# Performance work log

Measured on AMD Instinct MI355X. Metric: run time of the kernel, lower is better.

## Reference

```python
import jax, jax.numpy as jnp
import numpy as np

NEG_SLOPE = 0.2  # PyG GATConv default negative_slope
N_NODES = 50000


def gat_conv(x, src, dst, W, att_src, att_dst, bias, heads, out_ch):
    # x: [N, F_in]; src/dst: [E] (messages flow src -> dst, softmax over dst)
    N = x.shape[0]
    h = (x @ W).reshape(N, heads, out_ch)              # [N,H,C]
    a_src = jnp.sum(h * att_src, axis=-1)              # [N,H]
    a_dst = jnp.sum(h * att_dst, axis=-1)              # [N,H]
    e = jax.nn.leaky_relu(a_src[src] + a_dst[dst], NEG_SLOPE)   # [E,H]
    # numerically stable segment softmax over incoming edges of each dst node
    m = jax.ops.segment_max(e, dst, num_segments=N)    # [N,H]
    e = jnp.exp(e - m[dst])
    denom = jax.ops.segment_sum(e, dst, num_segments=N)
    alpha = e / (denom[dst] + 1e-16)                   # [E,H]
    msg = h[src] * alpha[:, :, None]                   # [E,H,C]
    out = jax.ops.segment_sum(msg, dst, num_segments=N)  # [N,H,C]
    return out.reshape(N, heads * out_ch) + bias


def add_self_loops(edge_index, num_nodes):
    loop = jnp.arange(num_nodes, dtype=edge_index.dtype)
    return jnp.concatenate([edge_index, jnp.stack([loop, loop])], axis=1)


def setup_inputs() -> dict:
    key = jax.random.key(0)
    ks = jax.random.split(key, 10)
    F_in, H, C, F_out = 256, 4, 64, 16
    x = jax.random.normal(ks[0], (N_NODES, F_in), dtype=jnp.float32)
    edge_index = jax.random.randint(ks[1], (2, 800000), 0, N_NODES, dtype=jnp.int64)
    s1 = 1.0 / np.sqrt(F_in)
    s2 = 1.0 / np.sqrt(H * C)
    return {
        "x": x,
        "edge_index": edge_index,
        "W1": jax.random.normal(ks[2], (F_in, H * C), dtype=jnp.float32) * s1,
        "att_src1": jax.random.normal(ks[3], (H, C), dtype=jnp.float32) * s2,
        "att_dst1": jax.random.normal(ks[4], (H, C), dtype=jnp.float32) * s2,
        "b1": jnp.zeros((H * C,), dtype=jnp.float32),
        "W2": jax.random.normal(ks[5], (H * C, F_out), dtype=jnp.float32) * s2,
        "att_src2": jax.random.normal(ks[6], (1, F_out), dtype=jnp.float32) * 0.25,
        "att_dst2": jax.random.normal(ks[7], (1, F_out), dtype=jnp.float32) * 0.25,
        "b2": jnp.zeros((F_out,), dtype=jnp.float32),
    }


def reference(x, edge_index, W1, att_src1, att_dst1, b1, W2, att_src2, att_dst2, b2):
    ei = add_self_loops(edge_index, x.shape[0])
    src, dst = ei[0], ei[1]
    H1, C1 = att_src1.shape
    h = gat_conv(x, src, dst, W1, att_src1, att_dst1, b1, H1, C1)
    h = jax.nn.relu(h)
    # F.dropout(training=False) is identity in eval mode
    H2, C2 = att_src2.shape
    out = gat_conv(h, src, dst, W2, att_src2, att_dst2, b2, H2, C2)
    return jax.nn.log_softmax(out, axis=1)
```

## Files before the change

kernel.cpp:

```cpp
#include <hip/hip_runtime.h>
#include <math.h>


typedef __attribute__((ext_vector_type(8))) short bf16x8;
typedef __attribute__((ext_vector_type(8))) unsigned short u16x8;
typedef __attribute__((ext_vector_type(4))) float f32x4;
typedef __attribute__((ext_vector_type(2))) float f32x2;

static __device__ inline unsigned short f2bf(float f) {
    unsigned u = __builtin_bit_cast(unsigned, f);
    unsigned r = (u + 0x7FFF + ((u >> 16) & 1)) >> 16;
    return (unsigned short)r;
}
static __device__ inline float bf2f(unsigned short u) {
    unsigned v = ((unsigned)u) << 16;
    return __builtin_bit_cast(float, v);
}
static __device__ inline float lrelu(float x) { return x > 0.f ? x : 0.2f * x; }

__global__ __launch_bounds__(256) void k_prep(const float* __restrict__ x,
                                              const float* __restrict__ W1,
                                              const float* __restrict__ b1,
                                              const float* __restrict__ W2,
                                              short* __restrict__ xb,
                                              unsigned short* __restrict__ csr,
                                              short* __restrict__ w1t,
                                              float* __restrict__ b1p,
                                              float* __restrict__ w2p,
                                              int* __restrict__ cnt,
                                              float* __restrict__ a1s,
                                              float* __restrict__ a2s,
                                              unsigned* __restrict__ h1f8u,
                                              float* __restrict__ h2,
                                              int N) {
    long idx = (long)blockIdx.x * 256 + threadIdx.x;
    const long T = (long)N * 32;
    if (idx < T) {
        const float* xp = x + idx * 8;
        float4 f0 = *(const float4*)xp;
        float4 f1 = *(const float4*)(xp + 4);
        short b[8];
        b[0] = (short)f2bf(f0.x); b[1] = (short)f2bf(f0.y);
        b[2] = (short)f2bf(f0.z); b[3] = (short)f2bf(f0.w);
        b[4] = (short)f2bf(f1.x); b[5] = (short)f2bf(f1.y);
        b[6] = (short)f2bf(f1.z); b[7] = (short)f2bf(f1.w);
        *(bf16x8*)(xb + idx * 8) = *(bf16x8*)&b[0];
    }
    if (idx < (long)N * 16) {
        ushort4 v = make_ushort4((unsigned short)N, (unsigned short)N,
                                 (unsigned short)N, (unsigned short)N);
        if ((idx & 15) == 0) v.x = (unsigned short)(idx >> 4);
        *(ushort4*)(csr + idx * 4) = v;
    }
    if (idx < N) cnt[idx] = 1;
    if (idx < 256) {
        int ct = ((int)idx >> 6) * 64 + ((int)idx & 3) * 16 + (((int)idx & 63) >> 2);
        b1p[idx] = b1[ct];
    }
    if (idx < 4096) {
        int pp = (int)idx >> 4, c2 = (int)idx & 15;
        int ct = (pp >> 6) * 64 + (pp & 3) * 16 + ((pp & 63) >> 2);
        w2p[idx] = W2[ct * 16 + c2];
    }
    if (idx < 4) a1s[(long)N * 4 + idx] = -1e30f;
    if (idx == 4) a2s[N] = -1e30f;
    if (idx < 64) h1f8u[(long)N * 64 + idx] = 0u;
    if (idx < 16) h2[(long)N * 16 + idx] = 0.f;
    if (idx < 65536) {
        int n = (int)idx >> 8, k = (int)idx & 255;
        w1t[n * 256 + k] = (short)f2bf(W1[k * 256 + n]);
    }
}

__global__ __launch_bounds__(256) void k_scatter(const int* __restrict__ ei,
                                                 int* __restrict__ cnt,
                                                 unsigned short* __restrict__ csr,
                                                 int E0) {
    int e0 = (blockIdx.x * 256 + threadIdx.x) << 3;
    if (e0 >= E0) return;
    if (e0 + 8 <= E0) {
        int4 sa = *(const int4*)&ei[e0];
        int4 sb = *(const int4*)&ei[e0 + 4];
        int4 da = *(const int4*)&ei[E0 + e0];
        int4 db = *(const int4*)&ei[E0 + e0 + 4];
        int ss[8] = {sa.x, sa.y, sa.z, sa.w, sb.x, sb.y, sb.z, sb.w};
        int dd[8] = {da.x, da.y, da.z, da.w, db.x, db.y, db.z, db.w};
        int sl[8];
#pragma unroll
        for (int q = 0; q < 8; ++q) sl[q] = atomicAdd(&cnt[dd[q]], 1);
#pragma unroll
        for (int q = 0; q < 8; ++q)
            if (sl[q] < 64) csr[((long)dd[q] << 6) + sl[q]] = (unsigned short)ss[q];
    } else {
        for (int e = e0; e < E0; ++e) {
            int s = ei[e], d = ei[E0 + e];
            int slot = atomicAdd(&cnt[d], 1);
            if (slot < 64) csr[((long)d << 6) + slot] = (unsigned short)s;
        }
    }
}

__global__ __launch_bounds__(256) void k_gemm1_mfma(const short* __restrict__ Ab,
                                                    const short* __restrict__ Bt,
                                                    const float* __restrict__ att_s,
                                                    const float* __restrict__ att_d,
                                                    unsigned char* __restrict__ C8,
                                                    float* __restrict__ a1s,
                                                    float* __restrict__ a1d,
                                                    int M) {
    __shared__ short As[64][40];
    __shared__ short Bs[128][40];
    const int bm = blockIdx.y * 64;
    const int bn = blockIdx.x * 128;
    const int tid = threadIdx.x;
    const int lane = tid & 63;
    const int wave = tid >> 6;
    const int wm = (wave >> 1) * 32;
    const int wn = (wave & 1) * 64;
    const int l15 = lane & 15;
    const int l4 = lane >> 4;

    const int ar = tid >> 2, aq = (tid & 3) * 8;
    const int br = tid >> 1, bh = (tid & 1) * 16;

    f32x4 acc[2][4] = {};

    for (int k0 = 0; k0 < 256; k0 += 32) {
        {
            bf16x8 av;
            if (bm + ar < M) {
                av = *(const bf16x8*)&Ab[(long)(bm + ar) * 256 + k0 + aq];
            } else {
#pragma unroll
                for (int q = 0; q < 8; ++q) av[q] = 0;
            }
            *(bf16x8*)&As[ar][aq] = av;
            const short* p = &Bt[(long)(bn + br) * 256 + k0 + bh];
            *(bf16x8*)&Bs[br][bh] = *(const bf16x8*)p;
            *(bf16x8*)&Bs[br][bh + 8] = *(const bf16x8*)(p + 8);
        }
        __syncthreads();

        bf16x8 af[2], bfr[4];
#pragma unroll
        for (int i = 0; i < 2; ++i)
            af[i] = *(const bf16x8*)&As[wm + i * 16 + l15][l4 * 8];
#pragma unroll
        for (int j = 0; j < 4; ++j)
            bfr[j] = *(const bf16x8*)&Bs[wn + j * 16 + l15][l4 * 8];
#pragma unroll
        for (int i = 0; i < 2; ++i)
#pragma unroll
            for (int j = 0; j < 4; ++j)
                acc[i][j] = __builtin_amdgcn_mfma_f32_16x16x32_bf16(af[i], bfr[j], acc[i][j], 0, 0, 0);
        __syncthreads();
    }

    const int h = (bn + wn) >> 6;
    float aws[4], awd[4];
#pragma unroll
    for (int j = 0; j < 4; ++j) {
        aws[j] = att_s[h * 64 + j * 16 + l15];
        awd[j] = att_d[h * 64 + j * 16 + l15];
    }

#pragma unroll
    for (int i = 0; i < 2; ++i) {
#pragma unroll
        for (int r = 0; r < 4; ++r) {
            float sv = 0.f, dv = 0.f;
#pragma unroll
            for (int j = 0; j < 4; ++j) {
                sv += acc[i][j][r] * aws[j];
                dv += acc[i][j][r] * awd[j];
            }
#pragma unroll
            for (int o = 1; o < 16; o <<= 1) {
                sv += __shfl_xor(sv, o);
                dv += __shfl_xor(dv, o);
            }
            int row = bm + wm + i * 16 + l4 * 4 + r;
            if (row < M) {
                if (l15 == 0) { a1s[row * 4 + h] = sv; a1d[row * 4 + h] = dv; }
                int d = 0;
                d = __builtin_amdgcn_cvt_pk_fp8_f32(acc[i][0][r], acc[i][1][r], d, false);
                d = __builtin_amdgcn_cvt_pk_fp8_f32(acc[i][2][r], acc[i][3][r], d, true);
                *(unsigned*)&C8[(long)row * 256 + (bn + wn) + l15 * 4] = (unsigned)d;
            }
        }
    }
}

__global__ __launch_bounds__(256) void k_gather1(const unsigned char* __restrict__ h1f8,
                                                 const int* __restrict__ cnt,
                                                 const unsigned short* __restrict__ csr,
                                                 const float* __restrict__ as1,
                                                 const float* __restrict__ ad1,
                                                 const float* __restrict__ b1p,
                                                 unsigned short* __restrict__ out1b,
                                                 int N) {
    int wid = blockIdx.x * 4 + (threadIdx.x >> 6);
    int lane = threadIdx.x & 63;
    if (wid >= N) return;

    const int es = lane >> 4;
    const int cl = lane & 15;
    const int hc = cl >> 2;
    const float adh = ad1[wid * 4 + hc];

    int c = min(cnt[wid], 64);
    int len4 = (c + 3) & ~3;
    const unsigned short* seg = csr + ((long)wid << 6);
    const char* as1c = (const char*)as1 + hc * 4;
    const char* h1c  = (const char*)h1f8 + cl * 16;

    float dacc = 0.f;
    f32x2 acc2[8] = {};
#pragma unroll 2
    for (int j0 = 0; j0 < len4; j0 += 4) {
        int sv = seg[j0 + es];
        float a = __expf(lrelu(*(const float*)(as1c + ((long)sv << 4)) + adh));
        dacc += a;
        f32x2 av = {a, a};
        uint4 v = *(const uint4*)(h1c + ((long)sv << 8));
        unsigned w[4] = {v.x, v.y, v.z, v.w};
#pragma unroll
        for (int q = 0; q < 4; ++q) {
            f32x2 lo = __builtin_amdgcn_cvt_pk_f32_fp8((int)w[q], false);
            f32x2 hi = __builtin_amdgcn_cvt_pk_f32_fp8((int)w[q], true);
            acc2[q * 2 + 0] += av * lo;
            acc2[q * 2 + 1] += av * hi;
        }
    }
    dacc += __shfl_xor(dacc, 16);
    dacc += __shfl_xor(dacc, 32);
    const float inv_c = 1.f / (dacc + 1e-16f);

    float accf[16];
#pragma unroll
    for (int q = 0; q < 8; ++q) { accf[2 * q] = acc2[q].x; accf[2 * q + 1] = acc2[q].y; }
#pragma unroll
    for (int q = 0; q < 16; ++q) {
        accf[q] += __shfl_xor(accf[q], 16);
        accf[q] += __shfl_xor(accf[q], 32);
    }
    if (lane < 16) {
        unsigned pk[8];
#pragma unroll
        for (int q = 0; q < 8; ++q) {
            float v0 = fmaxf(accf[q * 2 + 0] * inv_c + b1p[cl * 16 + q * 2 + 0], 0.f);
            float v1 = fmaxf(accf[q * 2 + 1] * inv_c + b1p[cl * 16 + q * 2 + 1], 0.f);
            pk[q] = (unsigned)f2bf(v0) | ((unsigned)f2bf(v1) << 16);
        }
        unsigned short* dst = &out1b[(long)wid * 256 + cl * 16];
        *(uint4*)dst = make_uint4(pk[0], pk[1], pk[2], pk[3]);
        *(uint4*)(dst + 8) = make_uint4(pk[4], pk[5], pk[6], pk[7]);
    }
}

__global__ __launch_bounds__(256) void k_gemm2(const unsigned short* __restrict__ Xb,
                                               const float* __restrict__ Wp,
                                               const float* __restrict__ att_s,
                                               const float* __restrict__ att_d,
                                               float* __restrict__ h2,
                                               float* __restrict__ a2s,
                                               float* __restrict__ a2d, int N) {
    __shared__ float Ws[256 * 16];
    for (int i = threadIdx.x; i < 1024; i += 256)
        ((float4*)Ws)[i] = ((const float4*)Wp)[i];
    __syncthreads();
    int r = threadIdx.x >> 4, c = threadIdx.x & 15;
    int row = blockIdx.x * 16 + r;
    if (row >= N) return;
    const unsigned short* xr = Xb + (long)row * 256;
    float acc = 0.f;
    for (int k = 0; k < 256; k += 8) {
        u16x8 xv = *(const u16x8*)&xr[k];
#pragma unroll
        for (int q = 0; q < 8; ++q)
            acc += bf2f(xv[q]) * Ws[(k + q) * 16 + c];
    }
    h2[row * 16 + c] = acc;
    float vs = acc * att_s[c];
    float vd = acc * att_d[c];
    for (int o = 1; o < 16; o <<= 1) { vs += __shfl_xor(vs, o); vd += __shfl_xor(vd, o); }
    if (c == 0) { a2s[row] = vs; a2d[row] = vd; }
}

__global__ __launch_bounds__(256) void k_gather2(const float* __restrict__ h2,
                                                 const int* __restrict__ cnt,
                                                 const unsigned short* __restrict__ csr,
                                                 const float* __restrict__ a2s,
                                                 const float* __restrict__ a2d,
                                                 const float* __restrict__ b2,
                                                 float* __restrict__ out, int N) {
    int wid = blockIdx.x * 4 + (threadIdx.x >> 6);
    int lane = threadIdx.x & 63;
    if (wid >= N) return;
    float adh = a2d[wid];
    const int es = lane >> 4;
    const int c = lane & 15;

    int cc = min(cnt[wid], 64);
    int len4 = (cc + 3) & ~3;
    const unsigned short* seg = csr + ((long)wid << 6);
    const char* a2c = (const char*)a2s;
    const char* h2c = (const char*)h2 + c * 4;

    float dacc = 0.f;
    float acc = 0.f;
#pragma unroll 2
    for (int j0 = 0; j0 < len4; j0 += 4) {
        int sv = seg[j0 + es];
        float a = __expf(lrelu(*(const float*)(a2c + ((long)sv << 2)) + adh));
        dacc += a;
        acc += a * *(const float*)(h2c + ((long)sv << 6));
    }
    acc += __shfl_xor(acc, 16);
    acc += __shfl_xor(acc, 32);
    dacc += __shfl_xor(dacc, 16);
    dacc += __shfl_xor(dacc, 32);
    float inv = 1.f / (dacc + 1e-16f);
    float v = acc * inv + b2[c];
    float mx = v;
    for (int o = 1; o < 16; o <<= 1) mx = fmaxf(mx, __shfl_xor(mx, o));
    float se = __expf(v - mx);
    for (int o = 1; o < 16; o <<= 1) se += __shfl_xor(se, o);
    float r = v - mx - logf(se);
    if (lane < 16) out[(long)wid * 16 + c] = r;
}

extern "C" void kernel_launch(void* const* d_in, const int* in_sizes, int n_in,
                              void* d_out, int out_size, void* d_ws, size_t ws_size,
                              hipStream_t stream) {
    const float* x    = (const float*)d_in[0];
    const int*   ei   = (const int*)d_in[1];
    const float* W1   = (const float*)d_in[2];
    const float* as1w = (const float*)d_in[3];
    const float* ad1w = (const float*)d_in[4];
    const float* b1   = (const float*)d_in[5];
    const float* W2   = (const float*)d_in[6];
    const float* as2w = (const float*)d_in[7];
    const float* ad2w = (const float*)d_in[8];
    const float* b2   = (const float*)d_in[9];
    float* out = (float*)d_out;

    const int N  = in_sizes[0] / 256;
    const int E0 = in_sizes[1] / 2;

    char* p = (char*)d_ws;
    unsigned char*  h1f8  = (unsigned char*)p;  p += (size_t)(N + 1) * 256;
    unsigned short* out1b = (unsigned short*)p; p += (size_t)N * 256 * sizeof(short);
    float* h2     = (float*)p; p += (size_t)(N + 1) * 16 * sizeof(float);
    float* a1s    = (float*)p; p += (size_t)(N + 1) * 4 * sizeof(float);
    float* a1d    = (float*)p; p += (size_t)N * 4 * sizeof(float);
    float* a2s    = (float*)p; p += (size_t)(N + 1) * sizeof(float);
    float* a2d    = (float*)p; p += (size_t)N * sizeof(float);
    float* b1p    = (float*)p; p += (size_t)256 * sizeof(float);
    float* w2p    = (float*)p; p += (size_t)4096 * sizeof(float);
    int*   cnt    = (int*)p;   p += (size_t)N * sizeof(int);
    short* w1t    = (short*)p; p += (size_t)256 * 256 * sizeof(short);
    unsigned short* csr = (unsigned short*)p; p += (size_t)N * 64 * sizeof(unsigned short);

    short* xb = (short*)out1b;

    const int NW = (N + 3) / 4;

    const long T = (long)N * 32;
    hipLaunchKernelGGL(k_prep, dim3((unsigned)((T + 255) / 256)), dim3(256), 0, stream,
                       x, W1, b1, W2, xb, csr, w1t, b1p, w2p, cnt, a1s, a2s,
                       (unsigned*)h1f8, h2, N);

    const int E8 = (E0 + 7) / 8;
    hipLaunchKernelGGL(k_scatter, dim3((E8 + 255) / 256), dim3(256), 0, stream,
                       ei, cnt, csr, E0);

    hipLaunchKernelGGL(k_gemm1_mfma, dim3(2, (N + 63) / 64), dim3(256), 0, stream,
                       xb, w1t, as1w, ad1w, h1f8, a1s, a1d, N);
    hipLaunchKernelGGL(k_gather1, dim3(NW), dim3(256), 0, stream,
                       h1f8, cnt, csr, a1s, a1d, b1p, out1b, N);

    hipLaunchKernelGGL(k_gemm2, dim3((N + 15) / 16), dim3(256), 0, stream,
                       out1b, w2p, as2w, ad2w, h2, a2s, a2d, N);
    hipLaunchKernelGGL(k_gather2, dim3(NW), dim3(256), 0, stream,
                       h2, cnt, csr, a2s, a2d, b2, out, N);
}
```

Baseline: 248.8 us.

## Build CSR via two-pass bucketed scatter with shared-memory histograms

```diff
diff --git a/kernel.cpp b/kernel.cpp
--- a/kernel.cpp
+++ b/kernel.cpp
@@ -6,6 +6,8 @@
 typedef __attribute__((ext_vector_type(8))) unsigned short u16x8;
 typedef __attribute__((ext_vector_type(4))) float f32x4;
 typedef __attribute__((ext_vector_type(2))) float f32x2;
+
+#define BCAP 1536
 
 static __device__ inline unsigned short f2bf(float f) {
     unsigned u = __builtin_bit_cast(unsigned, f);
@@ -27,12 +29,12 @@
                                               short* __restrict__ w1t,
                                               float* __restrict__ b1p,
                                               float* __restrict__ w2p,
-                                              int* __restrict__ cnt,
+                                              int* __restrict__ fill_bkt,
                                               float* __restrict__ a1s,
                                               float* __restrict__ a2s,
                                               unsigned* __restrict__ h1f8u,
                                               float* __restrict__ h2,
-                                              int N) {
+                                              int N, int nbuk) {
     long idx = (long)blockIdx.x * 256 + threadIdx.x;
     const long T = (long)N * 32;
     if (idx < T) {
@@ -52,7 +54,7 @@
         if ((idx & 15) == 0) v.x = (unsigned short)(idx >> 4);
         *(ushort4*)(csr + idx * 4) = v;
     }
-    if (idx < N) cnt[idx] = 1;
+    if (idx < nbuk) fill_bkt[idx] = 0;
     if (idx < 256) {
         int ct = ((int)idx >> 6) * 64 + ((int)idx & 3) * 16 + (((int)idx & 63) >> 2);
         b1p[idx] = b1[ct];
@@ -72,31 +74,66 @@
     }
 }
 
-__global__ __launch_bounds__(256) void k_scatter(const int* __restrict__ ei,
-                                                 int* __restrict__ cnt,
-                                                 unsigned short* __restrict__ csr,
-                                                 int E0) {
-    int e0 = (blockIdx.x * 256 + threadIdx.x) << 3;
-    if (e0 >= E0) return;
-    if (e0 + 8 <= E0) {
-        int4 sa = *(const int4*)&ei[e0];
-        int4 sb = *(const int4*)&ei[e0 + 4];
-        int4 da = *(const int4*)&ei[E0 + e0];
-        int4 db = *(const int4*)&ei[E0 + e0 + 4];
-        int ss[8] = {sa.x, sa.y, sa.z, sa.w, sb.x, sb.y, sb.z, sb.w};
-        int dd[8] = {da.x, da.y, da.z, da.w, db.x, db.y, db.z, db.w};
-        int sl[8];
-#pragma unroll
-        for (int q = 0; q < 8; ++q) sl[q] = atomicAdd(&cnt[dd[q]], 1);
-#pragma unroll
-        for (int q = 0; q < 8; ++q)
-            if (sl[q] < 64) csr[((long)dd[q] << 6) + sl[q]] = (unsigned short)ss[q];
-    } else {
-        for (int e = e0; e < E0; ++e) {
-            int s = ei[e], d = ei[E0 + e];
-            int slot = atomicAdd(&cnt[d], 1);
-            if (slot < 64) csr[((long)d << 6) + slot] = (unsigned short)s;
+__global__ __launch_bounds__(256) void k_bucketize(const int* __restrict__ ei,
+                                                   int* __restrict__ fill_bkt,
+                                                   unsigned* __restrict__ tmp,
+                                                   int E0, int nbuk) {
+    __shared__ int hist[1024];
+    __shared__ int base[1024];
+    const int t = threadIdx.x;
+    const int e0 = blockIdx.x * 4096;
+    for (int b = t; b < nbuk; b += 256) hist[b] = 0;
+    __syncthreads();
+    int ss[16], ds[16];
+    int nm = 0;
+#pragma unroll
+    for (int k = 0; k < 16; ++k) {
+        int e = e0 + t + k * 256;
+        if (e < E0) {
+            ss[nm] = ei[e];
+            ds[nm] = ei[E0 + e];
+            atomicAdd(&hist[ds[nm] >> 6], 1);
+            ++nm;
         }
+    }
+    __syncthreads();
+    for (int b = t; b < nbuk; b += 256) {
+        int c = hist[b];
+        base[b] = c ? atomicAdd(&fill_bkt[b], c) : 0;
+        hist[b] = 0;
+    }
+    __syncthreads();
+    for (int k = 0; k < nm; ++k) {
+        int b = ds[k] >> 6;
+        int r = base[b] + atomicAdd(&hist[b], 1);
+        if (r < BCAP)
+            tmp[(long)b * BCAP + r] = (unsigned)ss[k] | ((unsigned)(ds[k] & 63) << 16);
+    }
+}
+
+__global__ __launch_bounds__(256) void k_csr_fill2(const unsigned* __restrict__ tmp,
+                                                   const int* __restrict__ fill_bkt,
+                                                   int* __restrict__ cnt,
+                                                   unsigned short* __restrict__ csr,
+                                                   int N, int nbuk) {
+    __shared__ int lfill[64];
+    const int b = blockIdx.x;
+    const int t = threadIdx.x;
+    if (t < 64) lfill[t] = 0;
+    __syncthreads();
+    int c = min(fill_bkt[b], BCAP);
+    const unsigned* tp = tmp + (long)b * BCAP;
+    for (int i = t; i < c; i += 256) {
+        unsigned u = tp[i];
+        int dl = u >> 16;
+        int slot = atomicAdd(&lfill[dl], 1);
+        if (slot < 63)
+            csr[(((long)b * 64 + dl) << 6) + 1 + slot] = (unsigned short)(u & 0xffff);
+    }
+    __syncthreads();
+    if (t < 64) {
+        int d = b * 64 + t;
+        if (d < N) cnt[d] = 1 + min(lfill[t], 63);
     }
 }
 
@@ -345,8 +382,9 @@
     const float* b2   = (const float*)d_in[9];
     float* out = (float*)d_out;
 
-    const int N  = in_sizes[0] / 256;
-    const int E0 = in_sizes[1] / 2;
+    const int N    = in_sizes[0] / 256;
+    const int E0   = in_sizes[1] / 2;
+    const int NBUK = (N + 63) >> 6;
 
     char* p = (char*)d_ws;
     unsigned char*  h1f8  = (unsigned char*)p;  p += (size_t)(N + 1) * 256;
@@ -359,8 +397,10 @@
     float* b1p    = (float*)p; p += (size_t)256 * sizeof(float);
     float* w2p    = (float*)p; p += (size_t)4096 * sizeof(float);
     int*   cnt    = (int*)p;   p += (size_t)N * sizeof(int);
+    int*   fillbk = (int*)p;   p += (size_t)NBUK * sizeof(int);
     short* w1t    = (short*)p; p += (size_t)256 * 256 * sizeof(short);
     unsigned short* csr = (unsigned short*)p; p += (size_t)N * 64 * sizeof(unsigned short);
+    unsigned* tmp = (unsigned*)p; p += (size_t)NBUK * BCAP * sizeof(unsigned);
 
     short* xb = (short*)out1b;
 
@@ -368,12 +408,13 @@
 
     const long T = (long)N * 32;
     hipLaunchKernelGGL(k_prep, dim3((unsigned)((T + 255) / 256)), dim3(256), 0, stream,
-                       x, W1, b1, W2, xb, csr, w1t, b1p, w2p, cnt, a1s, a2s,
-                       (unsigned*)h1f8, h2, N);
-
-    const int E8 = (E0 + 7) / 8;
-    hipLaunchKernelGGL(k_scatter, dim3((E8 + 255) / 256), dim3(256), 0, stream,
-                       ei, cnt, csr, E0);
+                       x, W1, b1, W2, xb, csr, w1t, b1p, w2p, fillbk, a1s, a2s,
+                       (unsigned*)h1f8, h2, N, NBUK);
+
+    hipLaunchKernelGGL(k_bucketize, dim3((E0 + 4095) / 4096), dim3(256), 0, stream,
+                       ei, fillbk, tmp, E0, NBUK);
+    hipLaunchKernelGGL(k_csr_fill2, dim3(NBUK), dim3(256), 0, stream,
+                       tmp, fillbk, cnt, csr, N, NBUK);
 
     hipLaunchKernelGGL(k_gemm1_mfma, dim3(2, (N + 63) / 64), dim3(256), 0, stream,
                        xb, w1t, as1w, ad1w, h1f8, a1s, a1d, N);
```

After: 232.9 us. 1.07x faster.
